# Kernel optimization log

Hardware: AMD Instinct MI355X
Metric: run time of the kernel (lower is better)

The kernel has to match this reference:

```python
import jax, jax.numpy as jnp
import numpy as np

LN_EPS = 1e-5  # torch LayerNorm default
EPS = 1e-8     # slot-attention eps

def _ln(x, g, b):
    m = jnp.mean(x, axis=-1, keepdims=True)
    v = jnp.mean(jnp.square(x - m), axis=-1, keepdims=True)
    return (x - m) * jax.lax.rsqrt(v + LN_EPS) * g + b

def setup_inputs() -> dict:
    key = jax.random.key(0)
    ks = jax.random.split(key, 16)
    b, d, n_s, h = 131072, 256, 16, 256
    w_scale = d ** -0.5
    return {
        "inputs": jax.random.normal(ks[0], (b, 1, d), jnp.float32),
        "noise": jax.random.normal(ks[1], (n_s, d), jnp.float32),
        "slots_mu": jax.random.normal(ks[2], (1, d), jnp.float32),
        "slots_sigma": jax.random.uniform(ks[3], (1, d), jnp.float32),
        "Wq": jax.random.normal(ks[4], (d, d), jnp.float32) * w_scale,
        "bq": jnp.zeros((d,), jnp.float32),
        "Wk": jax.random.normal(ks[5], (d, d), jnp.float32) * w_scale,
        "bk": jnp.zeros((d,), jnp.float32),
        "Wv": jax.random.normal(ks[6], (d, d), jnp.float32) * w_scale,
        "bv": jnp.zeros((d,), jnp.float32),
        "W_ih": jax.random.normal(ks[7], (3 * d, d), jnp.float32) * w_scale,
        "W_hh": jax.random.normal(ks[8], (3 * d, d), jnp.float32) * w_scale,
        "b_ih": jnp.zeros((3 * d,), jnp.float32),
        "b_hh": jnp.zeros((3 * d,), jnp.float32),
        "W1": jax.random.normal(ks[9], (h, d), jnp.float32) * w_scale,
        "b1": jnp.zeros((h,), jnp.float32),
        "W2": jax.random.normal(ks[10], (d, h), jnp.float32) * (h ** -0.5),
        "b2": jnp.zeros((d,), jnp.float32),
        "g_in": jnp.ones((d,), jnp.float32),
        "be_in": jnp.zeros((d,), jnp.float32),
        "g_s": jnp.ones((d,), jnp.float32),
        "be_s": jnp.zeros((d,), jnp.float32),
        "g_f": jnp.ones((d,), jnp.float32),
        "be_f": jnp.zeros((d,), jnp.float32),
    }

def reference(inputs, noise, slots_mu, slots_sigma, Wq, bq, Wk, bk, Wv, bv,
              W_ih, W_hh, b_ih, b_hh, W1, b1, W2, b2,
              g_in, be_in, g_s, be_s, g_f, be_f):
    b, w, d = inputs.shape  # w == 1 required by the module's LayerNorm(dim)
    x = inputs.reshape(b, w * d)
    scale = d ** -0.5
    iters = 3

    slots = slots_mu + slots_sigma * noise  # (n_s, d), reparameterized normal

    x = _ln(x, g_in, be_in)
    k = x @ Wk.T + bk  # (b, d)
    v = x @ Wv.T + bv  # (b, d)

    for _ in range(iters):
        slots_prev = slots
        s = _ln(slots, g_s, be_s)
        q = s @ Wq.T + bq                      # (n_s, d)
        dots = jnp.einsum('nd,bd->nb', q, k) * scale
        attn = jax.nn.softmax(dots, axis=0) + EPS   # softmax over slots
        attn = attn / jnp.sum(attn, axis=-1, keepdims=True)
        updates = jnp.einsum('bd,nb->nd', v, attn)  # (n_s, d)
        # torch GRUCell
        gx = updates @ W_ih.T + b_ih                # (n_s, 3d)
        gh = slots_prev @ W_hh.T + b_hh
        xr, xz, xn = jnp.split(gx, 3, axis=-1)
        hr, hz, hn = jnp.split(gh, 3, axis=-1)
        r = jax.nn.sigmoid(xr + hr)
        z = jax.nn.sigmoid(xz + hz)
        n = jnp.tanh(xn + r * hn)
        slots = (1.0 - z) * n + z * slots_prev
        ff = jax.nn.relu(_ln(slots, g_f, be_f) @ W1.T + b1) @ W2.T + b2
        slots = slots + ff
    return slots
```

## Files before the change

### kernel.cpp

```cpp
#include <hip/hip_runtime.h>
#include <stdint.h>

#define B_ROWS 131072
#define SCALE 0.0625f
#define LN_EPS 1e-5f
#define ATTN_EPS 1e-8f

#define BIG_BLOCKS 512
#define ROWS_PER_BLOCK (B_ROWS / BIG_BLOCKS)
#define ROWS_PER_WAVE  (ROWS_PER_BLOCK / 4)
#define NSLICE BIG_BLOCKS

#define WS_PARTU 0
#define WS_PARTS (WS_PARTU + NSLICE*4096)
#define WS_U     (WS_PARTS + NSLICE*16)
#define WS_S     (WS_U + 4096)
#define WS_SLOTS (WS_S + 64)
#define WS_MID   (WS_SLOTS + 4096)
#define WS_GX    (WS_MID + 4096)
#define WS_GH    (WS_GX + 12288)
#define WS_H1    (WS_GH + 12288)
#define WS_QKG   (WS_H1 + 4096)
#define WS_QB    (WS_QKG + 4096)
#define WS_WIHV  (WS_QB + 64)
#define WS_BGX   (WS_WIHV + 196608)
#define WS_WQKG  (WS_BGX + 768)
#define WS_U2G   (WS_WQKG + 65536)
#define WS_U1    (WS_U2G + 256)
#define WS_C1    (WS_U1 + 256)

__global__ __launch_bounds__(256) void k_pre1(
    const float* __restrict__ Wq, const float* __restrict__ bq,
    const float* __restrict__ Wk, const float* __restrict__ bk,
    const float* __restrict__ Wv, const float* __restrict__ bv,
    const float* __restrict__ W_ih, const float* __restrict__ b_ih,
    const float* __restrict__ g_in, const float* __restrict__ be_in,
    float* __restrict__ ws)
{
  int bid = blockIdx.x, t = threadIdx.x;
  if (bid < 48) {
    int j0 = bid * 16;
    float acc[16];
#pragma unroll
    for (int r = 0; r < 16; r++) acc[r] = 0.f;
    int d = t;
    for (int dd = 0; dd < 256; dd++) {
      float v = Wv[dd * 256 + d];
#pragma unroll
      for (int r = 0; r < 16; r++)
        acc[r] = fmaf(W_ih[(j0 + r) * 256 + dd], v, acc[r]);
    }
#pragma unroll
    for (int r = 0; r < 16; r++) ws[WS_WIHV + (j0 + r) * 256 + d] = acc[r];
    if (t < 16) {
      int j = j0 + t;
      float a = b_ih[j];
      for (int dd = 0; dd < 256; dd++)
        a = fmaf(W_ih[j * 256 + dd], bv[dd], a);
      ws[WS_BGX + j] = a;
    }
  } else if (bid < 80) {
    int c0 = (bid - 48) * 8;
    float acc[8];
#pragma unroll
    for (int r = 0; r < 8; r++) acc[r] = 0.f;
    int d = t;
    for (int i = 0; i < 256; i++) {
      float wq = Wq[i * 256 + d];
#pragma unroll
      for (int r = 0; r < 8; r++)
        acc[r] = fmaf(wq, Wk[i * 256 + c0 + r], acc[r]);
    }
#pragma unroll
    for (int r = 0; r < 8; r++) {
      float gc = g_in[c0 + r];
      ws[WS_WQKG + (c0 + r) * 256 + d] = SCALE * gc * acc[r];
    }
    if (t < 8) {
      int c = c0 + t;
      float a = 0.f;
      for (int i = 0; i < 256; i++)
        a = fmaf(bq[i], Wk[i * 256 + c], a);
      ws[WS_U2G + c] = SCALE * g_in[c] * a;
    }
  } else {
    __shared__ __align__(16) float t2[256];
    int j = t;
    float a = 0.f;
    for (int dp = 0; dp < 256; dp++)
      a = fmaf(Wk[j * 256 + dp], be_in[dp], a);
    t2[j] = a + bk[j];
    __syncthreads();
    int d = t;
    float u = 0.f;
    for (int i = 0; i < 256; i++)
      u = fmaf(Wq[i * 256 + d], t2[i], u);
    ws[WS_U1 + d] = u;
    if (t == 0) {
      float c = 0.f;
      for (int i = 0; i < 256; i++) c = fmaf(bq[i], t2[i], c);
      ws[WS_C1] = c;
    }
  }
}

__global__ __launch_bounds__(256) void k_qkg(
    const float* __restrict__ noise, const float* __restrict__ mu,
    const float* __restrict__ sigma, const float* __restrict__ g_s,
    const float* __restrict__ be_s, float* __restrict__ ws, int init)
{
  __shared__ __align__(16) float sS[16 * 260];
  __shared__ __align__(16) float sAux[512];
  __shared__ __align__(16) float sStat[32];
  int bid = blockIdx.x, t = threadIdx.x;
  for (int n = 0; n < 16; n++) {
    float v;
    if (init) v = fmaf(sigma[t], noise[n * 256 + t], mu[t]);
    else      v = ws[WS_SLOTS + n * 256 + t];
    sS[n * 260 + t] = v;
    if (init && bid == 0) ws[WS_SLOTS + n * 256 + t] = v;
  }
  __syncthreads();
  { int n = t >> 4, c = t & 15;
    float s1 = 0.f, s2 = 0.f;
    for (int k = 0; k < 16; k++) {
      float x = sS[n * 260 + c * 16 + k];
      s1 += x; s2 = fmaf(x, x, s2);
    }
    sAux[n * 16 + c] = s1; sAux[256 + n * 16 + c] = s2; }
  __syncthreads();
  if (t < 16) {
    float s1 = 0.f, s2 = 0.f;
    for (int c = 0; c < 16; c++) { s1 += sAux[t * 16 + c]; s2 += sAux[256 + t * 16 + c]; }
    float m = s1 * (1.f / 256.f);
    float v = fmaxf(fmaf(-m, m, s2 * (1.f / 256.f)), 0.f);
    sStat[t] = m; sStat[16 + t] = rsqrtf(v + LN_EPS);
  }
  __syncthreads();
  { float gs = g_s[t], bs = be_s[t];
    for (int n = 0; n < 16; n++) {
      float m = sStat[n], rs = sStat[16 + n];
      sS[n * 260 + t] = fmaf((sS[n * 260 + t] - m) * rs, gs, bs);
    } }
  __syncthreads();
  if (bid < 64) {
    int cr = t >> 6, n = (t >> 2) & 15, ks = t & 3;
    int c = bid * 4 + cr;
    const float* wrow = ws + WS_WQKG + c * 256 + ks * 64;
    const float* srow = &sS[n * 260 + ks * 64];
    float acc = 0.f;
#pragma unroll
    for (int i = 0; i < 16; i++) {
      float4 w = *(const float4*)(wrow + i * 4);
      float4 s4 = *(const float4*)(srow + i * 4);
      acc = fmaf(w.x, s4.x, fmaf(w.y, s4.y, fmaf(w.z, s4.z, fmaf(w.w, s4.w, acc))));
    }
    sAux[t] = acc;
    __syncthreads();
    if (t < 64) {
      int cr2 = t >> 4, n2 = t & 15;
      int c2 = bid * 4 + cr2;
      int b = cr2 * 64 + n2 * 4;
      float s = sAux[b] + sAux[b + 1] + sAux[b + 2] + sAux[b + 3];
      ws[WS_QKG + n2 * 256 + c2] = s + ws[WS_U2G + c2];
    }
  } else {
    int n = t >> 4, ks = t & 15;
    float acc = 0.f;
    for (int k = 0; k < 16; k++)
      acc = fmaf(sS[n * 260 + ks * 16 + k], ws[WS_U1 + ks * 16 + k], acc);
    sAux[t] = acc;
    __syncthreads();
    if (t < 16) {
      float s = 0.f;
      for (int k = 0; k < 16; k++) s += sAux[t * 16 + k];
      ws[WS_QB + t] = SCALE * (s + ws[WS_C1]);
    }
  }
}

__global__ __launch_bounds__(256, 2) void k_big(
    const float* __restrict__ X, float* __restrict__ ws)
{
  __shared__ __align__(16) float red[4 * 4096];
  __shared__ __align__(16) float redS[64];
  int t = threadIdx.x;
  int wave = t >> 6, lane = t & 63;
  int p = lane >> 4, g = lane & 15;

  const float* qkg = ws + WS_QKG;
  float qw[4][16];
  float qs[4];
#pragma unroll
  for (int i = 0; i < 4; i++) {
    const float* rp = qkg + (4 * p + i) * 256 + g * 16;
#pragma unroll
    for (int jq = 0; jq < 4; jq++) {
      float4 v4 = *(const float4*)(rp + 4 * jq);
      qw[i][4 * jq + 0] = v4.x; qw[i][4 * jq + 1] = v4.y;
      qw[i][4 * jq + 2] = v4.z; qw[i][4 * jq + 3] = v4.w;
    }
    float s = 0.f;
#pragma unroll
    for (int j = 0; j < 16; j++) s += qw[i][j];
    qs[i] = s;
  }
#pragma unroll
  for (int m = 1; m <= 8; m <<= 1) {
#pragma unroll
    for (int i = 0; i < 4; i++) qs[i] += __shfl_xor(qs[i], m);
  }
  float qb0[4];
  {
    float4 q4 = *(const float4*)(ws + WS_QB + 4 * p);
    qb0[0] = q4.x; qb0[1] = q4.y; qb0[2] = q4.z; qb0[3] = q4.w;
  }

  float P[4][16];
#pragma unroll
  for (int i = 0; i < 4; i++)
#pragma unroll
    for (int j = 0; j < 16; j++) P[i][j] = 0.f;
  float Q[4] = {0.f, 0.f, 0.f, 0.f};
  float Sa[4] = {0.f, 0.f, 0.f, 0.f};

  size_t rowbase = (size_t)blockIdx.x * ROWS_PER_BLOCK + (size_t)wave * ROWS_PER_WAVE;
  const float* cur = X + rowbase * 256 + g * 16;
  float4 va = *(const float4*)cur;
  float4 vb = *(const float4*)(cur + 4);
  float4 vc = *(const float4*)(cur + 8);
  float4 vd = *(const float4*)(cur + 12);

#pragma unroll 1
  for (int r = 0; r < ROWS_PER_WAVE; r++) {
    const float* nxt = (r < ROWS_PER_WAVE - 1) ? (cur + 256) : cur;
    float4 na = *(const float4*)nxt;
    float4 nb = *(const float4*)(nxt + 4);
    float4 nc = *(const float4*)(nxt + 8);
    float4 nd = *(const float4*)(nxt + 12);

    float x[16];
    x[0] = va.x; x[1] = va.y; x[2] = va.z; x[3] = va.w;
    x[4] = vb.x; x[5] = vb.y; x[6] = vb.z; x[7] = vb.w;
    x[8] = vc.x; x[9] = vc.y; x[10] = vc.z; x[11] = vc.w;
    x[12] = vd.x; x[13] = vd.y; x[14] = vd.z; x[15] = vd.w;

    float s1 = 0.f, s2 = 0.f;
#pragma unroll
    for (int j = 0; j < 16; j++) { s1 += x[j]; s2 = fmaf(x[j], x[j], s2); }
#pragma unroll
    for (int m = 1; m <= 8; m <<= 1) {
      s1 += __shfl_xor(s1, m);
      s2 += __shfl_xor(s2, m);
    }
    float mean = s1 * (1.f / 256.f);
    float var = fmaxf(fmaf(-mean, mean, s2 * (1.f / 256.f)), 0.f);
    float rs = rsqrtf(var + LN_EPS);
    float mrs = mean * rs;

    float d0 = 0.f, d1 = 0.f, d2 = 0.f, d3 = 0.f;
#pragma unroll
    for (int j = 0; j < 16; j++) {
      d0 = fmaf(qw[0][j], x[j], d0);
      d1 = fmaf(qw[1][j], x[j], d1);
      d2 = fmaf(qw[2][j], x[j], d2);
      d3 = fmaf(qw[3][j], x[j], d3);
    }
#pragma unroll
    for (int m = 1; m <= 8; m <<= 1) {
      d0 += __shfl_xor(d0, m); d1 += __shfl_xor(d1, m);
      d2 += __shfl_xor(d2, m); d3 += __shfl_xor(d3, m);
    }
    float dsc[4];
    dsc[0] = fmaf(rs, d0, fmaf(-mrs, qs[0], qb0[0]));
    dsc[1] = fmaf(rs, d1, fmaf(-mrs, qs[1], qb0[1]));
    dsc[2] = fmaf(rs, d2, fmaf(-mrs, qs[2], qb0[2]));
    dsc[3] = fmaf(rs, d3, fmaf(-mrs, qs[3], qb0[3]));

    float mx = fmaxf(fmaxf(dsc[0], dsc[1]), fmaxf(dsc[2], dsc[3]));
    mx = fmaxf(mx, __shfl_xor(mx, 16));
    mx = fmaxf(mx, __shfl_xor(mx, 32));
    float e[4];
#pragma unroll
    for (int i = 0; i < 4; i++) e[i] = __expf(dsc[i] - mx);
    float se = e[0] + e[1] + e[2] + e[3];
    se += __shfl_xor(se, 16);
    se += __shfl_xor(se, 32);
    float inv = 1.0f / se;
    float a0[4], ar[4];
#pragma unroll
    for (int i = 0; i < 4; i++) {
      a0[i] = fmaf(e[i], inv, ATTN_EPS);
      ar[i] = a0[i] * rs;
    }
#pragma unroll
    for (int j = 0; j < 16; j++) {
      P[0][j] = fmaf(ar[0], x[j], P[0][j]);
      P[1][j] = fmaf(ar[1], x[j], P[1][j]);
      P[2][j] = fmaf(ar[2], x[j], P[2][j]);
      P[3][j] = fmaf(ar[3], x[j], P[3][j]);
    }
#pragma unroll
    for (int i = 0; i < 4; i++) {
      Q[i] = fmaf(a0[i], mrs, Q[i]);
      Sa[i] += a0[i];
    }
    va = na; vb = nb; vc = nc; vd = nd; cur = nxt;
  }

  if (g == 0) {
#pragma unroll
    for (int i = 0; i < 4; i++) redS[wave * 16 + 4 * p + i] = Sa[i];
  }
#pragma unroll
  for (int i = 0; i < 4; i++) {
#pragma unroll
    for (int jq = 0; jq < 4; jq++) {
      float4 v4;
      v4.x = P[i][4 * jq + 0] - Q[i]; v4.y = P[i][4 * jq + 1] - Q[i];
      v4.z = P[i][4 * jq + 2] - Q[i]; v4.w = P[i][4 * jq + 3] - Q[i];
      *(float4*)&red[wave * 4096 + (4 * p + i) * 256 + g * 16 + jq * 4] = v4;
    }
  }
  __syncthreads();
#pragma unroll
  for (int k = 0; k < 16; k++) {
    int idx = k * 256 + t;
    float v = red[idx] + red[4096 + idx] + red[8192 + idx] + red[12288 + idx];
    ws[WS_PARTU + (size_t)blockIdx.x * 4096 + idx] = v;
  }
  if (t < 16) {
    float sv = redS[t] + redS[16 + t] + redS[32 + t] + redS[48 + t];
    ws[WS_PARTS + blockIdx.x * 16 + t] = sv;
  }
}

__global__ __launch_bounds__(256) void k_red(float* __restrict__ ws)
{
  __shared__ __align__(16) float sAux[256];
  int bid = blockIdx.x, t = threadIdx.x;
  if (bid < 256) {
    int el = t & 15, wg = t >> 4;
    int e = bid * 16 + el;
    float acc = 0.f;
#pragma unroll 8
    for (int k = 0; k < 32; k++)
      acc += ws[WS_PARTU + (size_t)(wg + k * 16) * 4096 + e];
    sAux[t] = acc;
    __syncthreads();
    if (t < 16) {
      float s = 0.f;
      for (int w = 0; w < 16; w++) s += sAux[w * 16 + t];
      ws[WS_U + bid * 16 + t] = s;
    }
  } else {
    int n = t & 15, wg = t >> 4;
    float acc = 0.f;
#pragma unroll 8
    for (int k = 0; k < 32; k++)
      acc += ws[WS_PARTS + (wg + k * 16) * 16 + n];
    sAux[t] = acc;
    __syncthreads();
    if (t < 16) {
      float s = 0.f;
      for (int w = 0; w < 16; w++) s += sAux[w * 16 + t];
      ws[WS_S + t] = s;
    }
  }
}

__global__ __launch_bounds__(256) void k_gxgh(
    const float* __restrict__ W_hh, const float* __restrict__ b_hh,
    const float* __restrict__ g_in, const float* __restrict__ be_in,
    float* __restrict__ ws)
{
  __shared__ __align__(16) float sU[16 * 260];
  __shared__ __align__(16) float sInv[16];
  int bid = blockIdx.x, t = threadIdx.x;
  bool isgx = bid < 64;
  if (isgx && t < 16) sInv[t] = 1.0f / ws[WS_S + t];
  __syncthreads();
  if (isgx) {
    float gi = g_in[t], bi = be_in[t];
    for (int n = 0; n < 16; n++)
      sU[n * 260 + t] = fmaf(gi * ws[WS_U + n * 256 + t], sInv[n], bi);
  } else {
    for (int n = 0; n < 16; n++)
      sU[n * 260 + t] = ws[WS_SLOTS + n * 256 + t];
  }
  __syncthreads();
  int jr = t >> 4, n = t & 15;
  if (jr < 12) {
    int j = (isgx ? bid : bid - 64) * 12 + jr;
    const float* srow = &sU[n * 260];
    const float* wrow = isgx ? (ws + WS_WIHV + j * 256) : (W_hh + j * 256);
    float acc = isgx ? ws[WS_BGX + j] : b_hh[j];
#pragma unroll 8
    for (int k = 0; k < 64; k++) {
      float4 w = *(const float4*)(wrow + k * 4);
      float4 s4 = *(const float4*)(srow + k * 4);
      acc = fmaf(w.x, s4.x, fmaf(w.y, s4.y, fmaf(w.z, s4.z, fmaf(w.w, s4.w, acc))));
    }
    if (isgx) ws[WS_GX + n * 768 + j] = acc;
    else      ws[WS_GH + n * 768 + j] = acc;
  }
}

__global__ __launch_bounds__(256) void k_midh1(
    const float* __restrict__ W1, const float* __restrict__ b1,
    const float* __restrict__ g_f, const float* __restrict__ be_f,
    float* __restrict__ ws)
{
  __shared__ __align__(16) float sM[16 * 260];
  __shared__ __align__(16) float sAux[512];
  __shared__ __align__(16) float sStat[32];
  int bid = blockIdx.x, t = threadIdx.x;
  for (int n = 0; n < 16; n++) {
    float xr = ws[WS_GX + n * 768 + t],       hr = ws[WS_GH + n * 768 + t];
    float xz = ws[WS_GX + n * 768 + 256 + t], hz = ws[WS_GH + n * 768 + 256 + t];
    float xn = ws[WS_GX + n * 768 + 512 + t], hn = ws[WS_GH + n * 768 + 512 + t];
    float sp = ws[WS_SLOTS + n * 256 + t];
    float r = 1.f / (1.f + __expf(-(xr + hr)));
    float z = 1.f / (1.f + __expf(-(xz + hz)));
    float nn = tanhf(fmaf(r, hn, xn));
    float mid = fmaf(z, sp - nn, nn);
    sM[n * 260 + t] = mid;
    if (bid == 0) ws[WS_MID + n * 256 + t] = mid;
  }
  __syncthreads();
  { int n = t >> 4, c = t & 15;
    float s1 = 0.f, s2 = 0.f;
    for (int k = 0; k < 16; k++) {
      float x = sM[n * 260 + c * 16 + k];
      s1 += x; s2 = fmaf(x, x, s2);
    }
    sAux[n * 16 + c] = s1; sAux[256 + n * 16 + c] = s2; }
  __syncthreads();
  if (t < 16) {
    float s1 = 0.f, s2 = 0.f;
    for (int c = 0; c < 16; c++) { s1 += sAux[t * 16 + c]; s2 += sAux[256 + t * 16 + c]; }
    float m = s1 * (1.f / 256.f);
    float v = fmaxf(fmaf(-m, m, s2 * (1.f / 256.f)), 0.f);
    sStat[t] = m; sStat[16 + t] = rsqrtf(v + LN_EPS);
  }
  __syncthreads();
  { float gf = g_f[t], bf = be_f[t];
    for (int n = 0; n < 16; n++) {
      float m = sStat[n], rs = sStat[16 + n];
      sM[n * 260 + t] = fmaf((sM[n * 260 + t] - m) * rs, gf, bf);
    } }
  __syncthreads();
  int jr = t >> 6, n = (t >> 2) & 15, ks = t & 3;
  int j = bid * 4 + jr;
  const float* wrow = W1 + j * 256 + ks * 64;
  const float* srow = &sM[n * 260 + ks * 64];
  float acc = 0.f;
#pragma unroll
  for (int k = 0; k < 16; k++) {
    float4 w = *(const float4*)(wrow + k * 4);
    float4 s4 = *(const float4*)(srow + k * 4);
    acc = fmaf(w.x, s4.x, fmaf(w.y, s4.y, fmaf(w.z, s4.z, fmaf(w.w, s4.w, acc))));
  }
  sAux[t] = acc;
  __syncthreads();
  if (t < 64) {
    int jr2 = t >> 4, n2 = t & 15;
    int j2 = bid * 4 + jr2;
    int b = jr2 * 64 + n2 * 4;
    float s = sAux[b] + sAux[b + 1] + sAux[b + 2] + sAux[b + 3] + b1[j2];
    ws[WS_H1 + n2 * 256 + j2] = fmaxf(s, 0.f);
  }
}

__global__ __launch_bounds__(256) void k_ffnew(
    const float* __restrict__ W2, const float* __restrict__ b2v,
    float* __restrict__ out, float* __restrict__ ws)
{
  __shared__ __align__(16) float sH[16 * 260];
  __shared__ __align__(16) float sAux[256];
  int bid = blockIdx.x, t = threadIdx.x;
  for (int n = 0; n < 16; n++)
    sH[n * 260 + t] = ws[WS_H1 + n * 256 + t];
  __syncthreads();
  int dr = t >> 6, n = (t >> 2) & 15, ks = t & 3;
  int d = bid * 4 + dr;
  const float* wrow = W2 + d * 256 + ks * 64;
  const float* srow = &sH[n * 260 + ks * 64];
  float acc = 0.f;
#pragma unroll
  for (int k = 0; k < 16; k++) {
    float4 w = *(const float4*)(wrow + k * 4);
    float4 s4 = *(const float4*)(srow + k * 4);
    acc = fmaf(w.x, s4.x, fmaf(w.y, s4.y, fmaf(w.z, s4.z, fmaf(w.w, s4.w, acc))));
  }
  sAux[t] = acc;
  __syncthreads();
  if (t < 64) {
    int dr2 = t >> 4, n2 = t & 15;
    int d2 = bid * 4 + dr2;
    int b = dr2 * 64 + n2 * 4;
    float s = sAux[b] + sAux[b + 1] + sAux[b + 2] + sAux[b + 3]
            + b2v[d2] + ws[WS_MID + n2 * 256 + d2];
    ws[WS_SLOTS + n2 * 256 + d2] = s;
    out[n2 * 256 + d2] = s;
  }
}

extern "C" void kernel_launch(void* const* d_in, const int* in_sizes, int n_in,
                              void* d_out, int out_size, void* d_ws, size_t ws_size,
                              hipStream_t stream)
{
  (void)in_sizes; (void)n_in; (void)out_size; (void)ws_size;
  const float* inputs = (const float*)d_in[0];
  const float* noise  = (const float*)d_in[1];
  const float* mu     = (const float*)d_in[2];
  const float* sigma  = (const float*)d_in[3];
  const float* Wq     = (const float*)d_in[4];
  const float* bq     = (const float*)d_in[5];
  const float* Wk     = (const float*)d_in[6];
  const float* bk     = (const float*)d_in[7];
  const float* Wv     = (const float*)d_in[8];
  const float* bv     = (const float*)d_in[9];
  const float* W_ih   = (const float*)d_in[10];
  const float* W_hh   = (const float*)d_in[11];
  const float* b_ih   = (const float*)d_in[12];
  const float* b_hh   = (const float*)d_in[13];
  const float* W1     = (const float*)d_in[14];
  const float* b1     = (const float*)d_in[15];
  const float* W2     = (const float*)d_in[16];
  const float* b2     = (const float*)d_in[17];
  const float* g_in   = (const float*)d_in[18];
  const float* be_in  = (const float*)d_in[19];
  const float* g_s    = (const float*)d_in[20];
  const float* be_s   = (const float*)d_in[21];
  const float* g_f    = (const float*)d_in[22];
  const float* be_f   = (const float*)d_in[23];
  float* ws = (float*)d_ws;
  float* out = (float*)d_out;

  hipLaunchKernelGGL(k_pre1, dim3(81), dim3(256), 0, stream,
                     Wq, bq, Wk, bk, Wv, bv, W_ih, b_ih, g_in, be_in, ws);
  hipLaunchKernelGGL(k_qkg, dim3(65), dim3(256), 0, stream,
                     noise, mu, sigma, g_s, be_s, ws, 1);
  for (int it = 0; it < 3; it++) {
    hipLaunchKernelGGL(k_big, dim3(BIG_BLOCKS), dim3(256), 0, stream, inputs, ws);
    hipLaunchKernelGGL(k_red, dim3(257), dim3(256), 0, stream, ws);
    hipLaunchKernelGGL(k_gxgh, dim3(128), dim3(256), 0, stream,
                       W_hh, b_hh, g_in, be_in, ws);
    hipLaunchKernelGGL(k_midh1, dim3(64), dim3(256), 0, stream,
                       W1, b1, g_f, be_f, ws);
    hipLaunchKernelGGL(k_ffnew, dim3(64), dim3(256), 0, stream,
                       W2, b2, out, ws);
    if (it < 2)
      hipLaunchKernelGGL(k_qkg, dim3(65), dim3(256), 0, stream,
                         noise, mu, sigma, g_s, be_s, ws, 0);
  }
}
```

Baseline: 654.7 us.

## Fuse per-iteration slot kernels into one persistent kernel with grid barriers; widen k_big

Replaces the five small per-iteration kernels (reduce, gx/gh, GRU+FFN1, FFN2, q-projection) with one 128-block kernel that separates the stages with an atomic-counter grid barrier. This removes several kernel launch gaps per iteration. Separately, k_big now runs 512 threads per block (8 waves), and the extra waves are merged into the shared-memory reduction buffers. The barrier relies on all 128 blocks being resident at once, and the counter is reset inside k_pre1.

After: 1.353 ms. 2.07x slower.

```diff
diff --git a/kernel.cpp b/kernel.cpp
--- a/kernel.cpp
+++ b/kernel.cpp
@@ -7,8 +7,9 @@
 #define ATTN_EPS 1e-8f
 
 #define BIG_BLOCKS 512
+#define BIG_THREADS 512
 #define ROWS_PER_BLOCK (B_ROWS / BIG_BLOCKS)
-#define ROWS_PER_WAVE  (ROWS_PER_BLOCK / 4)
+#define ROWS_PER_WAVE  (ROWS_PER_BLOCK / 8)
 #define NSLICE BIG_BLOCKS
 
 #define WS_PARTU 0
@@ -28,6 +29,23 @@
 #define WS_U2G   (WS_WQKG + 65536)
 #define WS_U1    (WS_U2G + 256)
 #define WS_C1    (WS_U1 + 256)
+#define WS_CTR   (WS_C1 + 4)
+
+#define SLOT_BLOCKS 128u
+
+__device__ __forceinline__ void gridbar(unsigned int* ctr, unsigned int target)
+{
+  __syncthreads();
+  if (threadIdx.x == 0) {
+    __threadfence();
+    __hip_atomic_fetch_add(ctr, 1u, __ATOMIC_RELEASE, __HIP_MEMORY_SCOPE_AGENT);
+    while (__hip_atomic_load(ctr, __ATOMIC_RELAXED, __HIP_MEMORY_SCOPE_AGENT) < target) {
+      __builtin_amdgcn_s_sleep(1);
+    }
+    __threadfence();
+  }
+  __syncthreads();
+}
 
 __global__ __launch_bounds__(256) void k_pre1(
     const float* __restrict__ Wq, const float* __restrict__ bq,
@@ -85,6 +103,7 @@
     }
   } else {
     __shared__ __align__(16) float t2[256];
+    if (t == 0) *((unsigned int*)(ws + WS_CTR)) = 0u;
     int j = t;
     float a = 0.f;
     for (int dp = 0; dp < 256; dp++)
@@ -179,11 +198,11 @@
   }
 }
 
-__global__ __launch_bounds__(256, 2) void k_big(
+__global__ __launch_bounds__(512, 4) void k_big(
     const float* __restrict__ X, float* __restrict__ ws)
 {
   __shared__ __align__(16) float red[4 * 4096];
-  __shared__ __align__(16) float redS[64];
+  __shared__ __align__(16) float redS[128];
   int t = threadIdx.x;
   int wave = t >> 6, lane = t & 63;
   int p = lane >> 4, g = lane & 15;
@@ -308,201 +327,287 @@
     va = na; vb = nb; vc = nc; vd = nd; cur = nxt;
   }
 
+  int slot = wave & 3;
+  if (wave < 4) {
+#pragma unroll
+    for (int i = 0; i < 4; i++) {
+#pragma unroll
+      for (int jq = 0; jq < 4; jq++) {
+        float4 v4;
+        v4.x = P[i][4 * jq + 0] - Q[i]; v4.y = P[i][4 * jq + 1] - Q[i];
+        v4.z = P[i][4 * jq + 2] - Q[i]; v4.w = P[i][4 * jq + 3] - Q[i];
+        *(float4*)&red[slot * 4096 + (4 * p + i) * 256 + g * 16 + jq * 4] = v4;
+      }
+    }
+  }
   if (g == 0) {
 #pragma unroll
     for (int i = 0; i < 4; i++) redS[wave * 16 + 4 * p + i] = Sa[i];
   }
-#pragma unroll
-  for (int i = 0; i < 4; i++) {
-#pragma unroll
-    for (int jq = 0; jq < 4; jq++) {
-      float4 v4;
-      v4.x = P[i][4 * jq + 0] - Q[i]; v4.y = P[i][4 * jq + 1] - Q[i];
-      v4.z = P[i][4 * jq + 2] - Q[i]; v4.w = P[i][4 * jq + 3] - Q[i];
-      *(float4*)&red[wave * 4096 + (4 * p + i) * 256 + g * 16 + jq * 4] = v4;
-    }
-  }
-  __syncthreads();
-#pragma unroll
-  for (int k = 0; k < 16; k++) {
-    int idx = k * 256 + t;
+  __syncthreads();
+  if (wave >= 4) {
+#pragma unroll
+    for (int i = 0; i < 4; i++) {
+#pragma unroll
+      for (int jq = 0; jq < 4; jq++) {
+        float4* dst = (float4*)&red[slot * 4096 + (4 * p + i) * 256 + g * 16 + jq * 4];
+        float4 c = *dst;
+        c.x += P[i][4 * jq + 0] - Q[i]; c.y += P[i][4 * jq + 1] - Q[i];
+        c.z += P[i][4 * jq + 2] - Q[i]; c.w += P[i][4 * jq + 3] - Q[i];
+        *dst = c;
+      }
+    }
+  }
+  __syncthreads();
+#pragma unroll
+  for (int k = 0; k < 8; k++) {
+    int idx = k * 512 + t;
     float v = red[idx] + red[4096 + idx] + red[8192 + idx] + red[12288 + idx];
     ws[WS_PARTU + (size_t)blockIdx.x * 4096 + idx] = v;
   }
   if (t < 16) {
-    float sv = redS[t] + redS[16 + t] + redS[32 + t] + redS[48 + t];
+    float sv = 0.f;
+#pragma unroll
+    for (int w = 0; w < 8; w++) sv += redS[w * 16 + t];
     ws[WS_PARTS + blockIdx.x * 16 + t] = sv;
   }
 }
 
-__global__ __launch_bounds__(256) void k_red(float* __restrict__ ws)
+__global__ __launch_bounds__(256) void k_slot(
+    const float* __restrict__ W_hh, const float* __restrict__ b_hh,
+    const float* __restrict__ g_in, const float* __restrict__ be_in,
+    const float* __restrict__ W1, const float* __restrict__ b1,
+    const float* __restrict__ g_f, const float* __restrict__ be_f,
+    const float* __restrict__ W2, const float* __restrict__ b2v,
+    const float* __restrict__ g_s, const float* __restrict__ be_s,
+    float* __restrict__ out, float* __restrict__ ws, int it)
 {
-  __shared__ __align__(16) float sAux[256];
+  __shared__ __align__(16) float smem[4704];
+  float* sBuf  = smem;
+  float* sAux  = smem + 4160;
+  float* sStat = smem + 4672;
   int bid = blockIdx.x, t = threadIdx.x;
-  if (bid < 256) {
-    int el = t & 15, wg = t >> 4;
-    int e = bid * 16 + el;
+  unsigned int* ctr = (unsigned int*)(ws + WS_CTR);
+  unsigned int base = (unsigned int)it * 4u * SLOT_BLOCKS;
+
+  {
+    int le = t & 31, grp = t >> 5;
+    int e = bid * 32 + le;
     float acc = 0.f;
 #pragma unroll 8
-    for (int k = 0; k < 32; k++)
-      acc += ws[WS_PARTU + (size_t)(wg + k * 16) * 4096 + e];
+    for (int k = 0; k < 64; k++)
+      acc += ws[WS_PARTU + (size_t)(grp + k * 8) * 4096 + e];
     sAux[t] = acc;
     __syncthreads();
+    if (t < 32) {
+      float s = 0.f;
+#pragma unroll
+      for (int w = 0; w < 8; w++) s += sAux[w * 32 + t];
+      ws[WS_U + bid * 32 + t] = s;
+    }
+    if (bid == 0) {
+      int n = t & 15, g16 = t >> 4;
+      float a2 = 0.f;
+#pragma unroll 8
+      for (int k = 0; k < 32; k++)
+        a2 += ws[WS_PARTS + (g16 + k * 16) * 16 + n];
+      __syncthreads();
+      sAux[t] = a2;
+      __syncthreads();
+      if (t < 16) {
+        float s = 0.f;
+#pragma unroll
+        for (int w = 0; w < 16; w++) s += sAux[w * 16 + t];
+        ws[WS_S + t] = s;
+      }
+    }
+  }
+  gridbar(ctr, base + SLOT_BLOCKS);
+
+  {
+    bool isgx = bid < 64;
+    float* sU = sBuf;
+    float* sInv = sStat;
+    if (isgx && t < 16) sInv[t] = 1.0f / ws[WS_S + t];
+    __syncthreads();
+    if (isgx) {
+      float gi = g_in[t], bi = be_in[t];
+      for (int n = 0; n < 16; n++)
+        sU[n * 260 + t] = fmaf(gi * ws[WS_U + n * 256 + t], sInv[n], bi);
+    } else {
+      for (int n = 0; n < 16; n++)
+        sU[n * 260 + t] = ws[WS_SLOTS + n * 256 + t];
+    }
+    __syncthreads();
+    int jr = t >> 4, n = t & 15;
+    if (jr < 12) {
+      int j = (isgx ? bid : bid - 64) * 12 + jr;
+      const float* srow = &sU[n * 260];
+      const float* wrow = isgx ? (ws + WS_WIHV + j * 256) : (W_hh + j * 256);
+      float acc = isgx ? ws[WS_BGX + j] : b_hh[j];
+#pragma unroll 8
+      for (int k = 0; k < 64; k++) {
+        float4 w = *(const float4*)(wrow + k * 4);
+        float4 s4 = *(const float4*)(srow + k * 4);
+        acc = fmaf(w.x, s4.x, fmaf(w.y, s4.y, fmaf(w.z, s4.z, fmaf(w.w, s4.w, acc))));
+      }
+      if (isgx) ws[WS_GX + n * 768 + j] = acc;
+      else      ws[WS_GH + n * 768 + j] = acc;
+    }
+  }
+  gridbar(ctr, base + 2 * SLOT_BLOCKS);
+
+  if (bid < 64) {
+    float* sM = sBuf;
+    for (int n = 0; n < 16; n++) {
+      float xr = ws[WS_GX + n * 768 + t],       hr = ws[WS_GH + n * 768 + t];
+      float xz = ws[WS_GX + n * 768 + 256 + t], hz = ws[WS_GH + n * 768 + 256 + t];
+      float xn = ws[WS_GX + n * 768 + 512 + t], hn = ws[WS_GH + n * 768 + 512 + t];
+      float sp = ws[WS_SLOTS + n * 256 + t];
+      float r = 1.f / (1.f + __expf(-(xr + hr)));
+      float z = 1.f / (1.f + __expf(-(xz + hz)));
+      float nn = tanhf(fmaf(r, hn, xn));
+      float mid = fmaf(z, sp - nn, nn);
+      sM[n * 260 + t] = mid;
+      if (bid == 0) ws[WS_MID + n * 256 + t] = mid;
+    }
+    __syncthreads();
+    { int n = t >> 4, c = t & 15;
+      float s1 = 0.f, s2 = 0.f;
+      for (int k = 0; k < 16; k++) {
+        float x = sM[n * 260 + c * 16 + k];
+        s1 += x; s2 = fmaf(x, x, s2);
+      }
+      sAux[n * 16 + c] = s1; sAux[256 + n * 16 + c] = s2; }
+    __syncthreads();
     if (t < 16) {
-      float s = 0.f;
-      for (int w = 0; w < 16; w++) s += sAux[w * 16 + t];
-      ws[WS_U + bid * 16 + t] = s;
-    }
-  } else {
-    int n = t & 15, wg = t >> 4;
+      float s1 = 0.f, s2 = 0.f;
+      for (int c = 0; c < 16; c++) { s1 += sAux[t * 16 + c]; s2 += sAux[256 + t * 16 + c]; }
+      float m = s1 * (1.f / 256.f);
+      float v = fmaxf(fmaf(-m, m, s2 * (1.f / 256.f)), 0.f);
+      sStat[t] = m; sStat[16 + t] = rsqrtf(v + LN_EPS);
+    }
+    __syncthreads();
+    { float gf = g_f[t], bf = be_f[t];
+      for (int n = 0; n < 16; n++) {
+        float m = sStat[n], rs = sStat[16 + n];
+        sM[n * 260 + t] = fmaf((sM[n * 260 + t] - m) * rs, gf, bf);
+      } }
+    __syncthreads();
+    int jr = t >> 6, n = (t >> 2) & 15, ks = t & 3;
+    int j = bid * 4 + jr;
+    const float* wrow = W1 + j * 256 + ks * 64;
+    const float* srow = &sM[n * 260 + ks * 64];
     float acc = 0.f;
-#pragma unroll 8
-    for (int k = 0; k < 32; k++)
-      acc += ws[WS_PARTS + (wg + k * 16) * 16 + n];
-    sAux[t] = acc;
-    __syncthreads();
-    if (t < 16) {
-      float s = 0.f;
-      for (int w = 0; w < 16; w++) s += sAux[w * 16 + t];
-      ws[WS_S + t] = s;
-    }
-  }
-}
-
-__global__ __launch_bounds__(256) void k_gxgh(
-    const float* __restrict__ W_hh, const float* __restrict__ b_hh,
-    const float* __restrict__ g_in, const float* __restrict__ be_in,
-    float* __restrict__ ws)
-{
-  __shared__ __align__(16) float sU[16 * 260];
-  __shared__ __align__(16) float sInv[16];
-  int bid = blockIdx.x, t = threadIdx.x;
-  bool isgx = bid < 64;
-  if (isgx && t < 16) sInv[t] = 1.0f / ws[WS_S + t];
-  __syncthreads();
-  if (isgx) {
-    float gi = g_in[t], bi = be_in[t];
-    for (int n = 0; n < 16; n++)
-      sU[n * 260 + t] = fmaf(gi * ws[WS_U + n * 256 + t], sInv[n], bi);
-  } else {
-    for (int n = 0; n < 16; n++)
-      sU[n * 260 + t] = ws[WS_SLOTS + n * 256 + t];
-  }
-  __syncthreads();
-  int jr = t >> 4, n = t & 15;
-  if (jr < 12) {
-    int j = (isgx ? bid : bid - 64) * 12 + jr;
-    const float* srow = &sU[n * 260];
-    const float* wrow = isgx ? (ws + WS_WIHV + j * 256) : (W_hh + j * 256);
-    float acc = isgx ? ws[WS_BGX + j] : b_hh[j];
-#pragma unroll 8
-    for (int k = 0; k < 64; k++) {
+#pragma unroll
+    for (int k = 0; k < 16; k++) {
       float4 w = *(const float4*)(wrow + k * 4);
       float4 s4 = *(const float4*)(srow + k * 4);
       acc = fmaf(w.x, s4.x, fmaf(w.y, s4.y, fmaf(w.z, s4.z, fmaf(w.w, s4.w, acc))));
     }
-    if (isgx) ws[WS_GX + n * 768 + j] = acc;
-    else      ws[WS_GH + n * 768 + j] = acc;
-  }
-}
-
-__global__ __launch_bounds__(256) void k_midh1(
-    const float* __restrict__ W1, const float* __restrict__ b1,
-    const float* __restrict__ g_f, const float* __restrict__ be_f,
-    float* __restrict__ ws)
-{
-  __shared__ __align__(16) float sM[16 * 260];
-  __shared__ __align__(16) float sAux[512];
-  __shared__ __align__(16) float sStat[32];
-  int bid = blockIdx.x, t = threadIdx.x;
-  for (int n = 0; n < 16; n++) {
-    float xr = ws[WS_GX + n * 768 + t],       hr = ws[WS_GH + n * 768 + t];
-    float xz = ws[WS_GX + n * 768 + 256 + t], hz = ws[WS_GH + n * 768 + 256 + t];
-    float xn = ws[WS_GX + n * 768 + 512 + t], hn = ws[WS_GH + n * 768 + 512 + t];
-    float sp = ws[WS_SLOTS + n * 256 + t];
-    float r = 1.f / (1.f + __expf(-(xr + hr)));
-    float z = 1.f / (1.f + __expf(-(xz + hz)));
-    float nn = tanhf(fmaf(r, hn, xn));
-    float mid = fmaf(z, sp - nn, nn);
-    sM[n * 260 + t] = mid;
-    if (bid == 0) ws[WS_MID + n * 256 + t] = mid;
-  }
-  __syncthreads();
-  { int n = t >> 4, c = t & 15;
-    float s1 = 0.f, s2 = 0.f;
+    sAux[t] = acc;
+    __syncthreads();
+    if (t < 64) {
+      int jr2 = t >> 4, n2 = t & 15;
+      int j2 = bid * 4 + jr2;
+      int b = jr2 * 64 + n2 * 4;
+      float s = sAux[b] + sAux[b + 1] + sAux[b + 2] + sAux[b + 3] + b1[j2];
+      ws[WS_H1 + n2 * 256 + j2] = fmaxf(s, 0.f);
+    }
+  }
+  gridbar(ctr, base + 3 * SLOT_BLOCKS);
+
+  if (bid < 64) {
+    float* sH = sBuf;
+    for (int n = 0; n < 16; n++)
+      sH[n * 260 + t] = ws[WS_H1 + n * 256 + t];
+    __syncthreads();
+    int dr = t >> 6, n = (t >> 2) & 15, ks = t & 3;
+    int d = bid * 4 + dr;
+    const float* wrow = W2 + d * 256 + ks * 64;
+    const float* srow = &sH[n * 260 + ks * 64];
+    float acc = 0.f;
+#pragma unroll
     for (int k = 0; k < 16; k++) {
-      float x = sM[n * 260 + c * 16 + k];
-      s1 += x; s2 = fmaf(x, x, s2);
-    }
-    sAux[n * 16 + c] = s1; sAux[256 + n * 16 + c] = s2; }
-  __syncthreads();
-  if (t < 16) {
-    float s1 = 0.f, s2 = 0.f;
-    for (int c = 0; c < 16; c++) { s1 += sAux[t * 16 + c]; s2 += sAux[256 + t * 16 + c]; }
-    float m = s1 * (1.f / 256.f);
-    float v = fmaxf(fmaf(-m, m, s2 * (1.f / 256.f)), 0.f);
-    sStat[t] = m; sStat[16 + t] = rsqrtf(v + LN_EPS);
-  }
-  __syncthreads();
-  { float gf = g_f[t], bf = be_f[t];
-    for (int n = 0; n < 16; n++) {
-      float m = sStat[n], rs = sStat[16 + n];
-      sM[n * 260 + t] = fmaf((sM[n * 260 + t] - m) * rs, gf, bf);
-    } }
-  __syncthreads();
-  int jr = t >> 6, n = (t >> 2) & 15, ks = t & 3;
-  int j = bid * 4 + jr;
-  const float* wrow = W1 + j * 256 + ks * 64;
-  const float* srow = &sM[n * 260 + ks * 64];
-  float acc = 0.f;
-#pragma unroll
-  for (int k = 0; k < 16; k++) {
-    float4 w = *(const float4*)(wrow + k * 4);
-    float4 s4 = *(const float4*)(srow + k * 4);
-    acc = fmaf(w.x, s4.x, fmaf(w.y, s4.y, fmaf(w.z, s4.z, fmaf(w.w, s4.w, acc))));
-  }
-  sAux[t] = acc;
-  __syncthreads();
-  if (t < 64) {
-    int jr2 = t >> 4, n2 = t & 15;
-    int j2 = bid * 4 + jr2;
-    int b = jr2 * 64 + n2 * 4;
-    float s = sAux[b] + sAux[b + 1] + sAux[b + 2] + sAux[b + 3] + b1[j2];
-    ws[WS_H1 + n2 * 256 + j2] = fmaxf(s, 0.f);
-  }
-}
-
-__global__ __launch_bounds__(256) void k_ffnew(
-    const float* __restrict__ W2, const float* __restrict__ b2v,
-    float* __restrict__ out, float* __restrict__ ws)
-{
-  __shared__ __align__(16) float sH[16 * 260];
-  __shared__ __align__(16) float sAux[256];
-  int bid = blockIdx.x, t = threadIdx.x;
-  for (int n = 0; n < 16; n++)
-    sH[n * 260 + t] = ws[WS_H1 + n * 256 + t];
-  __syncthreads();
-  int dr = t >> 6, n = (t >> 2) & 15, ks = t & 3;
-  int d = bid * 4 + dr;
-  const float* wrow = W2 + d * 256 + ks * 64;
-  const float* srow = &sH[n * 260 + ks * 64];
-  float acc = 0.f;
-#pragma unroll
-  for (int k = 0; k < 16; k++) {
-    float4 w = *(const float4*)(wrow + k * 4);
-    float4 s4 = *(const float4*)(srow + k * 4);
-    acc = fmaf(w.x, s4.x, fmaf(w.y, s4.y, fmaf(w.z, s4.z, fmaf(w.w, s4.w, acc))));
-  }
-  sAux[t] = acc;
-  __syncthreads();
-  if (t < 64) {
-    int dr2 = t >> 4, n2 = t & 15;
-    int d2 = bid * 4 + dr2;
-    int b = dr2 * 64 + n2 * 4;
-    float s = sAux[b] + sAux[b + 1] + sAux[b + 2] + sAux[b + 3]
-            + b2v[d2] + ws[WS_MID + n2 * 256 + d2];
-    ws[WS_SLOTS + n2 * 256 + d2] = s;
-    out[n2 * 256 + d2] = s;
+      float4 w = *(const float4*)(wrow + k * 4);
+      float4 s4 = *(const float4*)(srow + k * 4);
+      acc = fmaf(w.x, s4.x, fmaf(w.y, s4.y, fmaf(w.z, s4.z, fmaf(w.w, s4.w, acc))));
+    }
+    sAux[t] = acc;
+    __syncthreads();
+    if (t < 64) {
+      int dr2 = t >> 4, n2 = t & 15;
+      int d2 = bid * 4 + dr2;
+      int b = dr2 * 64 + n2 * 4;
+      float s = sAux[b] + sAux[b + 1] + sAux[b + 2] + sAux[b + 3]
+              + b2v[d2] + ws[WS_MID + n2 * 256 + d2];
+      ws[WS_SLOTS + n2 * 256 + d2] = s;
+      out[n2 * 256 + d2] = s;
+    }
+  }
+  gridbar(ctr, base + 4 * SLOT_BLOCKS);
+
+  if (it < 2 && bid <= 64) {
+    float* sS = sBuf;
+    for (int n = 0; n < 16; n++)
+      sS[n * 260 + t] = ws[WS_SLOTS + n * 256 + t];
+    __syncthreads();
+    { int n = t >> 4, c = t & 15;
+      float s1 = 0.f, s2 = 0.f;
+      for (int k = 0; k < 16; k++) {
+        float x = sS[n * 260 + c * 16 + k];
+        s1 += x; s2 = fmaf(x, x, s2);
+      }
+      sAux[n * 16 + c] = s1; sAux[256 + n * 16 + c] = s2; }
+    __syncthreads();
+    if (t < 16) {
+      float s1 = 0.f, s2 = 0.f;
+      for (int c = 0; c < 16; c++) { s1 += sAux[t * 16 + c]; s2 += sAux[256 + t * 16 + c]; }
+      float m = s1 * (1.f / 256.f);
+      float v = fmaxf(fmaf(-m, m, s2 * (1.f / 256.f)), 0.f);
+      sStat[t] = m; sStat[16 + t] = rsqrtf(v + LN_EPS);
+    }
+    __syncthreads();
+    { float gs = g_s[t], bs = be_s[t];
+      for (int n = 0; n < 16; n++) {
+        float m = sStat[n], rs = sStat[16 + n];
+        sS[n * 260 + t] = fmaf((sS[n * 260 + t] - m) * rs, gs, bs);
+      } }
+    __syncthreads();
+    if (bid < 64) {
+      int cr = t >> 6, n = (t >> 2) & 15, ks = t & 3;
+      int c = bid * 4 + cr;
+      const float* wrow = ws + WS_WQKG + c * 256 + ks * 64;
+      const float* srow = &sS[n * 260 + ks * 64];
+      float acc = 0.f;
+#pragma unroll
+      for (int i = 0; i < 16; i++) {
+        float4 w = *(const float4*)(wrow + i * 4);
+        float4 s4 = *(const float4*)(srow + i * 4);
+        acc = fmaf(w.x, s4.x, fmaf(w.y, s4.y, fmaf(w.z, s4.z, fmaf(w.w, s4.w, acc))));
+      }
+      sAux[t] = acc;
+      __syncthreads();
+      if (t < 64) {
+        int cr2 = t >> 4, n2 = t & 15;
+        int c2 = bid * 4 + cr2;
+        int b = cr2 * 64 + n2 * 4;
+        float s = sAux[b] + sAux[b + 1] + sAux[b + 2] + sAux[b + 3];
+        ws[WS_QKG + n2 * 256 + c2] = s + ws[WS_U2G + c2];
+      }
+    } else {
+      int n = t >> 4, ks = t & 15;
+      float acc = 0.f;
+      for (int k = 0; k < 16; k++)
+        acc = fmaf(sS[n * 260 + ks * 16 + k], ws[WS_U1 + ks * 16 + k], acc);
+      sAux[t] = acc;
+      __syncthreads();
+      if (t < 16) {
+        float s = 0.f;
+        for (int k = 0; k < 16; k++) s += sAux[t * 16 + k];
+        ws[WS_QB + t] = SCALE * (s + ws[WS_C1]);
+      }
+    }
   }
 }
 
@@ -543,16 +648,9 @@
   hipLaunchKernelGGL(k_qkg, dim3(65), dim3(256), 0, stream,
                      noise, mu, sigma, g_s, be_s, ws, 1);
   for (int it = 0; it < 3; it++) {
-    hipLaunchKernelGGL(k_big, dim3(BIG_BLOCKS), dim3(256), 0, stream, inputs, ws);
-    hipLaunchKernelGGL(k_red, dim3(257), dim3(256), 0, stream, ws);
-    hipLaunchKernelGGL(k_gxgh, dim3(128), dim3(256), 0, stream,
-                       W_hh, b_hh, g_in, be_in, ws);
-    hipLaunchKernelGGL(k_midh1, dim3(64), dim3(256), 0, stream,
-                       W1, b1, g_f, be_f, ws);
-    hipLaunchKernelGGL(k_ffnew, dim3(64), dim3(256), 0, stream,
-                       W2, b2, out, ws);
-    if (it < 2)
-      hipLaunchKernelGGL(k_qkg, dim3(65), dim3(256), 0, stream,
-                         noise, mu, sigma, g_s, be_s, ws, 0);
+    hipLaunchKernelGGL(k_big, dim3(BIG_BLOCKS), dim3(BIG_THREADS), 0, stream, inputs, ws);
+    hipLaunchKernelGGL(k_slot, dim3(SLOT_BLOCKS), dim3(256), 0, stream,
+                       W_hh, b_hh, g_in, be_in, W1, b1, g_f, be_f,
+                       W2, b2, g_s, be_s, out, ws, it);
   }
 }
```

## Double k_big block size and process two rows per loop iteration

Applied to the files above, without the earlier changes.

k_big now runs 512 threads (8 waves) per block, each wave handling half as many rows, and the inner loop handles two rows per iteration with a two-row prefetch so more independent work and memory traffic is in flight. The block reduction is reworked so waves 4-7 add into the shared buffers written by waves 0-3, which costs an extra barrier. The two-row body raises register pressure (x0/x1, prefetch registers, duplicated temporaries) while launch bounds of 512x2 tighten the per-thread register budget, which may cause spills.

New measurement: 634.6 us. 3.1% less time.

```diff
diff --git a/kernel.cpp b/kernel.cpp
--- a/kernel.cpp
+++ b/kernel.cpp
@@ -7,8 +7,9 @@
 #define ATTN_EPS 1e-8f
 
 #define BIG_BLOCKS 512
+#define BIG_THREADS 512
 #define ROWS_PER_BLOCK (B_ROWS / BIG_BLOCKS)
-#define ROWS_PER_WAVE  (ROWS_PER_BLOCK / 4)
+#define ROWS_PER_WAVE  (ROWS_PER_BLOCK / 8)
 #define NSLICE BIG_BLOCKS
 
 #define WS_PARTU 0
@@ -179,11 +180,11 @@
   }
 }
 
-__global__ __launch_bounds__(256, 2) void k_big(
+__global__ __launch_bounds__(512, 2) void k_big(
     const float* __restrict__ X, float* __restrict__ ws)
 {
   __shared__ __align__(16) float red[4 * 4096];
-  __shared__ __align__(16) float redS[64];
+  __shared__ __align__(16) float redS[128];
   int t = threadIdx.x;
   int wave = t >> 6, lane = t & 63;
   int p = lane >> 4, g = lane & 15;
@@ -225,112 +226,165 @@
   float Sa[4] = {0.f, 0.f, 0.f, 0.f};
 
   size_t rowbase = (size_t)blockIdx.x * ROWS_PER_BLOCK + (size_t)wave * ROWS_PER_WAVE;
-  const float* cur = X + rowbase * 256 + g * 16;
-  float4 va = *(const float4*)cur;
-  float4 vb = *(const float4*)(cur + 4);
-  float4 vc = *(const float4*)(cur + 8);
-  float4 vd = *(const float4*)(cur + 12);
+  const float* base = X + rowbase * 256 + g * 16;
+
+  float4 cA0 = *(const float4*)(base + 0);
+  float4 cB0 = *(const float4*)(base + 4);
+  float4 cC0 = *(const float4*)(base + 8);
+  float4 cD0 = *(const float4*)(base + 12);
+  float4 cA1 = *(const float4*)(base + 256);
+  float4 cB1 = *(const float4*)(base + 260);
+  float4 cC1 = *(const float4*)(base + 264);
+  float4 cD1 = *(const float4*)(base + 268);
 
 #pragma unroll 1
-  for (int r = 0; r < ROWS_PER_WAVE; r++) {
-    const float* nxt = (r < ROWS_PER_WAVE - 1) ? (cur + 256) : cur;
-    float4 na = *(const float4*)nxt;
-    float4 nb = *(const float4*)(nxt + 4);
-    float4 nc = *(const float4*)(nxt + 8);
-    float4 nd = *(const float4*)(nxt + 12);
-
-    float x[16];
-    x[0] = va.x; x[1] = va.y; x[2] = va.z; x[3] = va.w;
-    x[4] = vb.x; x[5] = vb.y; x[6] = vb.z; x[7] = vb.w;
-    x[8] = vc.x; x[9] = vc.y; x[10] = vc.z; x[11] = vc.w;
-    x[12] = vd.x; x[13] = vd.y; x[14] = vd.z; x[15] = vd.w;
-
-    float s1 = 0.f, s2 = 0.f;
-#pragma unroll
-    for (int j = 0; j < 16; j++) { s1 += x[j]; s2 = fmaf(x[j], x[j], s2); }
+  for (int r = 0; r < ROWS_PER_WAVE; r += 2) {
+    const float* nx = base + (size_t)((r + 2 < ROWS_PER_WAVE) ? (r + 2) : 0) * 256;
+    float4 pA0 = *(const float4*)(nx + 0);
+    float4 pB0 = *(const float4*)(nx + 4);
+    float4 pC0 = *(const float4*)(nx + 8);
+    float4 pD0 = *(const float4*)(nx + 12);
+    float4 pA1 = *(const float4*)(nx + 256);
+    float4 pB1 = *(const float4*)(nx + 260);
+    float4 pC1 = *(const float4*)(nx + 264);
+    float4 pD1 = *(const float4*)(nx + 268);
+
+    float x0[16], x1[16];
+    x0[0] = cA0.x; x0[1] = cA0.y; x0[2] = cA0.z; x0[3] = cA0.w;
+    x0[4] = cB0.x; x0[5] = cB0.y; x0[6] = cB0.z; x0[7] = cB0.w;
+    x0[8] = cC0.x; x0[9] = cC0.y; x0[10] = cC0.z; x0[11] = cC0.w;
+    x0[12] = cD0.x; x0[13] = cD0.y; x0[14] = cD0.z; x0[15] = cD0.w;
+    x1[0] = cA1.x; x1[1] = cA1.y; x1[2] = cA1.z; x1[3] = cA1.w;
+    x1[4] = cB1.x; x1[5] = cB1.y; x1[6] = cB1.z; x1[7] = cB1.w;
+    x1[8] = cC1.x; x1[9] = cC1.y; x1[10] = cC1.z; x1[11] = cC1.w;
+    x1[12] = cD1.x; x1[13] = cD1.y; x1[14] = cD1.z; x1[15] = cD1.w;
+
+    float s10 = 0.f, s20 = 0.f, s11 = 0.f, s21 = 0.f;
+#pragma unroll
+    for (int j = 0; j < 16; j++) {
+      s10 += x0[j]; s20 = fmaf(x0[j], x0[j], s20);
+      s11 += x1[j]; s21 = fmaf(x1[j], x1[j], s21);
+    }
 #pragma unroll
     for (int m = 1; m <= 8; m <<= 1) {
-      s1 += __shfl_xor(s1, m);
-      s2 += __shfl_xor(s2, m);
-    }
-    float mean = s1 * (1.f / 256.f);
-    float var = fmaxf(fmaf(-mean, mean, s2 * (1.f / 256.f)), 0.f);
-    float rs = rsqrtf(var + LN_EPS);
-    float mrs = mean * rs;
-
-    float d0 = 0.f, d1 = 0.f, d2 = 0.f, d3 = 0.f;
+      s10 += __shfl_xor(s10, m); s11 += __shfl_xor(s11, m);
+      s20 += __shfl_xor(s20, m); s21 += __shfl_xor(s21, m);
+    }
+    float mean0 = s10 * (1.f / 256.f), mean1 = s11 * (1.f / 256.f);
+    float var0 = fmaxf(fmaf(-mean0, mean0, s20 * (1.f / 256.f)), 0.f);
+    float var1 = fmaxf(fmaf(-mean1, mean1, s21 * (1.f / 256.f)), 0.f);
+    float rs0 = rsqrtf(var0 + LN_EPS), rs1 = rsqrtf(var1 + LN_EPS);
+    float mrs0 = mean0 * rs0, mrs1 = mean1 * rs1;
+
+    float d0[4] = {0.f, 0.f, 0.f, 0.f};
+    float d1[4] = {0.f, 0.f, 0.f, 0.f};
 #pragma unroll
     for (int j = 0; j < 16; j++) {
-      d0 = fmaf(qw[0][j], x[j], d0);
-      d1 = fmaf(qw[1][j], x[j], d1);
-      d2 = fmaf(qw[2][j], x[j], d2);
-      d3 = fmaf(qw[3][j], x[j], d3);
+#pragma unroll
+      for (int i = 0; i < 4; i++) {
+        d0[i] = fmaf(qw[i][j], x0[j], d0[i]);
+        d1[i] = fmaf(qw[i][j], x1[j], d1[i]);
+      }
     }
 #pragma unroll
     for (int m = 1; m <= 8; m <<= 1) {
-      d0 += __shfl_xor(d0, m); d1 += __shfl_xor(d1, m);
-      d2 += __shfl_xor(d2, m); d3 += __shfl_xor(d3, m);
-    }
-    float dsc[4];
-    dsc[0] = fmaf(rs, d0, fmaf(-mrs, qs[0], qb0[0]));
-    dsc[1] = fmaf(rs, d1, fmaf(-mrs, qs[1], qb0[1]));
-    dsc[2] = fmaf(rs, d2, fmaf(-mrs, qs[2], qb0[2]));
-    dsc[3] = fmaf(rs, d3, fmaf(-mrs, qs[3], qb0[3]));
-
-    float mx = fmaxf(fmaxf(dsc[0], dsc[1]), fmaxf(dsc[2], dsc[3]));
-    mx = fmaxf(mx, __shfl_xor(mx, 16));
-    mx = fmaxf(mx, __shfl_xor(mx, 32));
-    float e[4];
-#pragma unroll
-    for (int i = 0; i < 4; i++) e[i] = __expf(dsc[i] - mx);
-    float se = e[0] + e[1] + e[2] + e[3];
-    se += __shfl_xor(se, 16);
-    se += __shfl_xor(se, 32);
-    float inv = 1.0f / se;
-    float a0[4], ar[4];
+#pragma unroll
+      for (int i = 0; i < 4; i++) {
+        d0[i] += __shfl_xor(d0[i], m);
+        d1[i] += __shfl_xor(d1[i], m);
+      }
+    }
+    float dsc0[4], dsc1[4];
 #pragma unroll
     for (int i = 0; i < 4; i++) {
-      a0[i] = fmaf(e[i], inv, ATTN_EPS);
-      ar[i] = a0[i] * rs;
-    }
+      dsc0[i] = fmaf(rs0, d0[i], fmaf(-mrs0, qs[i], qb0[i]));
+      dsc1[i] = fmaf(rs1, d1[i], fmaf(-mrs1, qs[i], qb0[i]));
+    }
+
+    float mx0 = fmaxf(fmaxf(dsc0[0], dsc0[1]), fmaxf(dsc0[2], dsc0[3]));
+    float mx1 = fmaxf(fmaxf(dsc1[0], dsc1[1]), fmaxf(dsc1[2], dsc1[3]));
+    mx0 = fmaxf(mx0, __shfl_xor(mx0, 16)); mx1 = fmaxf(mx1, __shfl_xor(mx1, 16));
+    mx0 = fmaxf(mx0, __shfl_xor(mx0, 32)); mx1 = fmaxf(mx1, __shfl_xor(mx1, 32));
+    float e0[4], e1[4];
+#pragma unroll
+    for (int i = 0; i < 4; i++) {
+      e0[i] = __expf(dsc0[i] - mx0);
+      e1[i] = __expf(dsc1[i] - mx1);
+    }
+    float se0 = e0[0] + e0[1] + e0[2] + e0[3];
+    float se1 = e1[0] + e1[1] + e1[2] + e1[3];
+    se0 += __shfl_xor(se0, 16); se1 += __shfl_xor(se1, 16);
+    se0 += __shfl_xor(se0, 32); se1 += __shfl_xor(se1, 32);
+    float inv0 = 1.0f / se0, inv1 = 1.0f / se1;
+    float a0v[4], ar0[4], a1v[4], ar1[4];
+#pragma unroll
+    for (int i = 0; i < 4; i++) {
+      a0v[i] = fmaf(e0[i], inv0, ATTN_EPS); ar0[i] = a0v[i] * rs0;
+      a1v[i] = fmaf(e1[i], inv1, ATTN_EPS); ar1[i] = a1v[i] * rs1;
+    }
+
 #pragma unroll
     for (int j = 0; j < 16; j++) {
-      P[0][j] = fmaf(ar[0], x[j], P[0][j]);
-      P[1][j] = fmaf(ar[1], x[j], P[1][j]);
-      P[2][j] = fmaf(ar[2], x[j], P[2][j]);
-      P[3][j] = fmaf(ar[3], x[j], P[3][j]);
+#pragma unroll
+      for (int i = 0; i < 4; i++) {
+        P[i][j] = fmaf(ar0[i], x0[j], P[i][j]);
+        P[i][j] = fmaf(ar1[i], x1[j], P[i][j]);
+      }
     }
 #pragma unroll
     for (int i = 0; i < 4; i++) {
-      Q[i] = fmaf(a0[i], mrs, Q[i]);
-      Sa[i] += a0[i];
-    }
-    va = na; vb = nb; vc = nc; vd = nd; cur = nxt;
-  }
-
+      Q[i] = fmaf(a0v[i], mrs0, Q[i]);
+      Q[i] = fmaf(a1v[i], mrs1, Q[i]);
+      Sa[i] += a0v[i];
+      Sa[i] += a1v[i];
+    }
+
+    cA0 = pA0; cB0 = pB0; cC0 = pC0; cD0 = pD0;
+    cA1 = pA1; cB1 = pB1; cC1 = pC1; cD1 = pD1;
+  }
+
+  int slot = wave & 3;
+  if (wave < 4) {
+#pragma unroll
+    for (int i = 0; i < 4; i++) {
+#pragma unroll
+      for (int jq = 0; jq < 4; jq++) {
+        float4 v4;
+        v4.x = P[i][4 * jq + 0] - Q[i]; v4.y = P[i][4 * jq + 1] - Q[i];
+        v4.z = P[i][4 * jq + 2] - Q[i]; v4.w = P[i][4 * jq + 3] - Q[i];
+        *(float4*)&red[slot * 4096 + (4 * p + i) * 256 + g * 16 + jq * 4] = v4;
+      }
+    }
+  }
   if (g == 0) {
 #pragma unroll
     for (int i = 0; i < 4; i++) redS[wave * 16 + 4 * p + i] = Sa[i];
   }
-#pragma unroll
-  for (int i = 0; i < 4; i++) {
-#pragma unroll
-    for (int jq = 0; jq < 4; jq++) {
-      float4 v4;
-      v4.x = P[i][4 * jq + 0] - Q[i]; v4.y = P[i][4 * jq + 1] - Q[i];
-      v4.z = P[i][4 * jq + 2] - Q[i]; v4.w = P[i][4 * jq + 3] - Q[i];
-      *(float4*)&red[wave * 4096 + (4 * p + i) * 256 + g * 16 + jq * 4] = v4;
-    }
-  }
-  __syncthreads();
-#pragma unroll
-  for (int k = 0; k < 16; k++) {
-    int idx = k * 256 + t;
+  __syncthreads();
+  if (wave >= 4) {
+#pragma unroll
+    for (int i = 0; i < 4; i++) {
+#pragma unroll
+      for (int jq = 0; jq < 4; jq++) {
+        float4* dst = (float4*)&red[slot * 4096 + (4 * p + i) * 256 + g * 16 + jq * 4];
+        float4 c = *dst;
+        c.x += P[i][4 * jq + 0] - Q[i]; c.y += P[i][4 * jq + 1] - Q[i];
+        c.z += P[i][4 * jq + 2] - Q[i]; c.w += P[i][4 * jq + 3] - Q[i];
+        *dst = c;
+      }
+    }
+  }
+  __syncthreads();
+#pragma unroll
+  for (int k = 0; k < 8; k++) {
+    int idx = k * 512 + t;
     float v = red[idx] + red[4096 + idx] + red[8192 + idx] + red[12288 + idx];
     ws[WS_PARTU + (size_t)blockIdx.x * 4096 + idx] = v;
   }
   if (t < 16) {
-    float sv = redS[t] + redS[16 + t] + redS[32 + t] + redS[48 + t];
+    float sv = 0.f;
+#pragma unroll
+    for (int w = 0; w < 8; w++) sv += redS[w * 16 + t];
     ws[WS_PARTS + blockIdx.x * 16 + t] = sv;
   }
 }
@@ -543,7 +597,7 @@
   hipLaunchKernelGGL(k_qkg, dim3(65), dim3(256), 0, stream,
                      noise, mu, sigma, g_s, be_s, ws, 1);
   for (int it = 0; it < 3; it++) {
-    hipLaunchKernelGGL(k_big, dim3(BIG_BLOCKS), dim3(256), 0, stream, inputs, ws);
+    hipLaunchKernelGGL(k_big, dim3(BIG_BLOCKS), dim3(BIG_THREADS), 0, stream, inputs, ws);
     hipLaunchKernelGGL(k_red, dim3(257), dim3(256), 0, stream, ws);
     hipLaunchKernelGGL(k_gxgh, dim3(128), dim3(256), 0, stream,
                        W_hh, b_hh, g_in, be_in, ws);
```
